# Performance work log

Hardware: AMD Instinct MI355X
Metric: run time of the kernel (lower is better)

The kernel has to match this reference:

```python
import jax, jax.numpy as jnp
import numpy as np


def reference(key, value, time_decay, time_first):
    # key, value: [B, T, H]; time_decay/time_first: [H]
    u = time_first
    w = -jnp.exp(time_decay)
    B, T, H = key.shape

    def step(carry, kv):
        a, b, exponent = carry  # each [B, H]
        kt, vt = kv             # [B, H] each
        # numerically stabilized WKV output at this timestep
        max_e = jnp.maximum(exponent, u + kt)
        wt = jnp.exp(u + kt - max_e)
        scale = jnp.exp(exponent - max_e)
        wkv = (a * scale + wt * vt) / (b * scale + wt)
        # state update with decay w
        max_e2 = jnp.maximum(exponent + w, kt)
        s1 = jnp.exp(exponent + w - max_e2)
        s2 = jnp.exp(kt - max_e2)
        a_new = s1 * a + s2 * vt
        b_new = s1 * b + s2
        return (a_new, b_new, max_e2), wkv

    init = (
        jnp.zeros((B, H), dtype=key.dtype),
        jnp.zeros((B, H), dtype=key.dtype),
        jnp.full((B, H), -jnp.inf, dtype=key.dtype),
    )
    k_t = jnp.transpose(key, (1, 0, 2))    # [T, B, H]
    v_t = jnp.transpose(value, (1, 0, 2))  # [T, B, H]
    _, out = jax.lax.scan(step, init, (k_t, v_t))
    return jnp.transpose(out, (1, 0, 2))   # [B, T, H]


def setup_inputs() -> dict:
    k = jax.random.key(0)
    k1, k2, k3, k4 = jax.random.split(k, 4)
    B, T, H = 8, 2048, 768
    return {
        "key": jax.random.normal(k1, (B, T, H), dtype=jnp.float32),
        "value": jax.random.normal(k2, (B, T, H), dtype=jnp.float32),
        "time_decay": jax.random.normal(k3, (H,), dtype=jnp.float32),
        "time_first": jax.random.normal(k4, (H,), dtype=jnp.float32),
    }
```

## Files before the change

kernel.cpp:

```cpp
#include <hip/hip_runtime.h>
#include <math.h>


#define B_    8
#define T_    2048
#define H_    768
#define H4_   (H_/4)
#define NQ_   8
#define NCB_  32
#define L_    8
#define QLEN_ (NCB_*L_)
#define HS_   (H_/32)
#define HO4_  8
#define NT_   256
#define PAD_  33

#define EXCL_N ((size_t)B_*HS_*NQ_*NCB_*32)
#define TOT_N  ((size_t)B_*HS_*NQ_*32)

__global__ __launch_bounds__(NT_) void wkv_p1(
    const float* __restrict__ key, const float* __restrict__ val,
    const float* __restrict__ time_decay,
    float* __restrict__ ea, float* __restrict__ eb, float* __restrict__ ee,
    float* __restrict__ ta, float* __restrict__ tb, float* __restrict__ te)
{
    __shared__ float sa[NCB_][PAD_];
    __shared__ float sb[NCB_][PAD_];
    __shared__ float se[NCB_][PAD_];

    const int tid = threadIdx.x;
    const int ho4 = tid & (HO4_ - 1);
    const int c   = tid >> 3;
    const int col = ho4 * 4;
    const int hs  = blockIdx.x;
    const int q   = blockIdx.y;
    const int b   = blockIdx.z;
    const int h0  = hs * 32 + col;

    const float4 td4 = *(const float4*)(time_decay + h0);
    float w[4];
    w[0] = -__expf(td4.x); w[1] = -__expf(td4.y);
    w[2] = -__expf(td4.z); w[3] = -__expf(td4.w);

    const int cg = q * NCB_ + c;
    const size_t base = ((size_t)b * T_ + (size_t)cg * L_) * H_ + h0;
    const float4* kp = (const float4*)(key + base);
    const float4* vp = (const float4*)(val + base);

    float4 kr[L_], vr[L_];
#pragma unroll
    for (int t = 0; t < L_; ++t) {
        kr[t] = kp[(size_t)t * H4_];
        vr[t] = vp[(size_t)t * H4_];
    }

    float a[4]  = {0.f, 0.f, 0.f, 0.f};
    float bb[4] = {0.f, 0.f, 0.f, 0.f};
    float e[4]  = {-INFINITY, -INFINITY, -INFINITY, -INFINITY};

#pragma unroll
    for (int t = 0; t < L_; ++t) {
        const float kt[4] = {kr[t].x, kr[t].y, kr[t].z, kr[t].w};
        const float vt[4] = {vr[t].x, vr[t].y, vr[t].z, vr[t].w};
#pragma unroll
        for (int j = 0; j < 4; ++j) {
            const float ew = e[j] + w[j];
            const float m2 = fmaxf(ew, kt[j]);
            const float s1 = __expf(ew - m2);
            const float s2 = __expf(kt[j] - m2);
            a[j]  = fmaf(s1, a[j],  s2 * vt[j]);
            bb[j] = fmaf(s1, bb[j], s2);
            e[j]  = m2;
        }
    }

#pragma unroll
    for (int j = 0; j < 4; ++j) {
        sa[c][col + j] = a[j];
        sb[c][col + j] = bb[j];
        se[c][col + j] = e[j];
    }
    __syncthreads();

#pragma unroll
    for (int s = 0; s < 5; ++s) {
        const int d = 1 << s;
        const bool act = (c >= d);
        float pa[4], pb[4], pe[4];
        if (act) {
#pragma unroll
            for (int j = 0; j < 4; ++j) {
                pa[j] = sa[c - d][col + j];
                pb[j] = sb[c - d][col + j];
                pe[j] = se[c - d][col + j] + w[j] * (float)(L_ * d);
            }
        }
        __syncthreads();
        if (act) {
#pragma unroll
            for (int j = 0; j < 4; ++j) {
                const float m = fmaxf(pe[j], e[j]);
                const float x = __expf(pe[j] - m);
                const float y = __expf(e[j] - m);
                a[j]  = fmaf(pa[j], x, a[j] * y);
                bb[j] = fmaf(pb[j], x, bb[j] * y);
                e[j]  = m;
                sa[c][col + j] = a[j];
                sb[c][col + j] = bb[j];
                se[c][col + j] = e[j];
            }
        }
        __syncthreads();
    }

    float xa[4] = {0.f, 0.f, 0.f, 0.f};
    float xb[4] = {0.f, 0.f, 0.f, 0.f};
    float xe[4] = {-INFINITY, -INFINITY, -INFINITY, -INFINITY};
    if (c > 0) {
#pragma unroll
        for (int j = 0; j < 4; ++j) {
            xa[j] = sa[c - 1][col + j];
            xb[j] = sb[c - 1][col + j];
            xe[j] = se[c - 1][col + j];
        }
    }

    const size_t eoff = ((((size_t)b * HS_ + hs) * NQ_ + q) * NCB_ + c) * 32 + col;
#pragma unroll
    for (int j = 0; j < 4; ++j) {
        ea[eoff + j] = xa[j];
        eb[eoff + j] = xb[j];
        ee[eoff + j] = xe[j];
    }
    if (c == NCB_ - 1) {
        const size_t toff = (((size_t)b * HS_ + hs) * NQ_ + q) * 32 + col;
#pragma unroll
        for (int j = 0; j < 4; ++j) {
            ta[toff + j] = a[j];
            tb[toff + j] = bb[j];
            te[toff + j] = e[j];
        }
    }
}

__global__ __launch_bounds__(NT_) void wkv_p2(
    const float* __restrict__ key, const float* __restrict__ val,
    const float* __restrict__ time_decay, const float* __restrict__ time_first,
    const float* __restrict__ ea, const float* __restrict__ eb,
    const float* __restrict__ ee,
    const float* __restrict__ ta, const float* __restrict__ tb,
    const float* __restrict__ te,
    float* __restrict__ out)
{
    const int tid = threadIdx.x;
    const int ho4 = tid & (HO4_ - 1);
    const int c   = tid >> 3;
    const int col = ho4 * 4;
    const int hs  = blockIdx.x;
    const int q   = blockIdx.y;
    const int b   = blockIdx.z;
    const int h0  = hs * 32 + col;

    const int cg = q * NCB_ + c;
    const size_t base = ((size_t)b * T_ + (size_t)cg * L_) * H_ + h0;
    const float4* kp = (const float4*)(key + base);
    const float4* vp = (const float4*)(val + base);

    float4 kr[L_], vr[L_];
#pragma unroll
    for (int t = 0; t < L_; ++t) {
        kr[t] = kp[(size_t)t * H4_];
        vr[t] = vp[(size_t)t * H4_];
    }

    const float4 td4 = *(const float4*)(time_decay + h0);
    const float4 tf4 = *(const float4*)(time_first + h0);
    float w[4], u[4];
    w[0] = -__expf(td4.x); w[1] = -__expf(td4.y);
    w[2] = -__expf(td4.z); w[3] = -__expf(td4.w);
    u[0] = tf4.x; u[1] = tf4.y; u[2] = tf4.z; u[3] = tf4.w;

    const size_t eoff = ((((size_t)b * HS_ + hs) * NQ_ + q) * NCB_ + c) * 32 + col;
    float ra[4], rb[4], re[4];
#pragma unroll
    for (int j = 0; j < 4; ++j) {
        ra[j] = ea[eoff + j];
        rb[j] = eb[eoff + j];
        re[j] = ee[eoff + j];
    }

    float pa[4] = {0.f, 0.f, 0.f, 0.f};
    float pb[4] = {0.f, 0.f, 0.f, 0.f};
    float pe[4] = {-INFINITY, -INFINITY, -INFINITY, -INFINITY};
    for (int qq = 0; qq < q; ++qq) {
        const size_t toff = (((size_t)b * HS_ + hs) * NQ_ + qq) * 32 + col;
#pragma unroll
        for (int j = 0; j < 4; ++j) {
            const float Ta = ta[toff + j];
            const float Tb = tb[toff + j];
            const float Te = te[toff + j];
            const float sh = pe[j] + w[j] * (float)QLEN_;
            const float m  = fmaxf(sh, Te);
            const float x  = __expf(sh - m);
            const float y  = __expf(Te - m);
            pa[j] = fmaf(pa[j], x, Ta * y);
            pb[j] = fmaf(pb[j], x, Tb * y);
            pe[j] = m;
        }
    }

#pragma unroll
    for (int j = 0; j < 4; ++j) {
        const float sh = pe[j] + w[j] * (float)(c * L_);
        const float m  = fmaxf(sh, re[j]);
        if (m > -INFINITY) {
            const float x = __expf(sh - m);
            const float y = __expf(re[j] - m);
            ra[j] = fmaf(pa[j], x, ra[j] * y);
            rb[j] = fmaf(pb[j], x, rb[j] * y);
            re[j] = m;
        }
    }

    float4* op = (float4*)(out + base);
#pragma unroll
    for (int t = 0; t < L_; ++t) {
        const float kt[4] = {kr[t].x, kr[t].y, kr[t].z, kr[t].w};
        const float vt[4] = {vr[t].x, vr[t].y, vr[t].z, vr[t].w};
        float o[4];
#pragma unroll
        for (int j = 0; j < 4; ++j) {
            const float uk = u[j] + kt[j];
            const float m1 = fmaxf(re[j], uk);
            const float wt = __expf(uk - m1);
            const float sc = __expf(re[j] - m1);
            const float num = fmaf(ra[j], sc, wt * vt[j]);
            const float den = fmaf(rb[j], sc, wt);
            o[j] = __fdividef(num, den);

            const float ew = re[j] + w[j];
            const float m2 = fmaxf(ew, kt[j]);
            const float s1 = __expf(ew - m2);
            const float s2 = __expf(kt[j] - m2);
            ra[j] = fmaf(s1, ra[j], s2 * vt[j]);
            rb[j] = fmaf(s1, rb[j], s2);
            re[j] = m2;
        }
        float4 o4;
        o4.x = o[0]; o4.y = o[1]; o4.z = o[2]; o4.w = o[3];
        op[(size_t)t * H4_] = o4;
    }
}

extern "C" void kernel_launch(void* const* d_in, const int* in_sizes, int n_in,
                              void* d_out, int out_size, void* d_ws, size_t ws_size,
                              hipStream_t stream) {
    const float* key = (const float*)d_in[0];
    const float* val = (const float*)d_in[1];
    const float* td  = (const float*)d_in[2];
    const float* tf  = (const float*)d_in[3];
    float* out = (float*)d_out;

    float* ea = (float*)d_ws;
    float* eb = ea + EXCL_N;
    float* ee = eb + EXCL_N;
    float* ta = ee + EXCL_N;
    float* tb = ta + TOT_N;
    float* te = tb + TOT_N;

    dim3 grid(HS_, NQ_, B_);
    wkv_p1<<<grid, NT_, 0, stream>>>(key, val, td, ea, eb, ee, ta, tb, te);
    wkv_p2<<<grid, NT_, 0, stream>>>(key, val, td, tf, ea, eb, ee, ta, tb, te, out);
}
```

Before: 171.2 us.

## Process two sequence chunks per block and use lgkm-only barriers

Each block now handles two consecutive 256-step chunks instead of one, halving the grid and issuing loads for both chunks up front so the second chunk's global loads overlap the first chunk's compute. __syncthreads is replaced with an inline-asm barrier that waits only on LDS counters, so outstanding global loads need not drain at each scan step. The cost is double the register footprint for the key/value buffers and half as many blocks, which may cut occupancy and parallelism on a 256-CU device.

New measurement: 177.4 us. 1.04x slower.

```diff
diff --git a/kernel.cpp b/kernel.cpp
--- a/kernel.cpp
+++ b/kernel.cpp
@@ -18,42 +18,16 @@
 #define EXCL_N ((size_t)B_*HS_*NQ_*NCB_*32)
 #define TOT_N  ((size_t)B_*HS_*NQ_*32)
 
-__global__ __launch_bounds__(NT_) void wkv_p1(
-    const float* __restrict__ key, const float* __restrict__ val,
-    const float* __restrict__ time_decay,
+#define BAR_LGKM() asm volatile("s_waitcnt lgkmcnt(0)\n\ts_barrier" ::: "memory")
+
+__device__ __forceinline__ void k1_tile(
+    float (*sa)[PAD_], float (*sb)[PAD_], float (*se)[PAD_],
+    const float4* kr, const float4* vr, const float* w,
+    const int c, const int col,
     float* __restrict__ ea, float* __restrict__ eb, float* __restrict__ ee,
-    float* __restrict__ ta, float* __restrict__ tb, float* __restrict__ te)
+    float* __restrict__ ta, float* __restrict__ tb, float* __restrict__ te,
+    const size_t eoff, const size_t toff)
 {
-    __shared__ float sa[NCB_][PAD_];
-    __shared__ float sb[NCB_][PAD_];
-    __shared__ float se[NCB_][PAD_];
-
-    const int tid = threadIdx.x;
-    const int ho4 = tid & (HO4_ - 1);
-    const int c   = tid >> 3;
-    const int col = ho4 * 4;
-    const int hs  = blockIdx.x;
-    const int q   = blockIdx.y;
-    const int b   = blockIdx.z;
-    const int h0  = hs * 32 + col;
-
-    const float4 td4 = *(const float4*)(time_decay + h0);
-    float w[4];
-    w[0] = -__expf(td4.x); w[1] = -__expf(td4.y);
-    w[2] = -__expf(td4.z); w[3] = -__expf(td4.w);
-
-    const int cg = q * NCB_ + c;
-    const size_t base = ((size_t)b * T_ + (size_t)cg * L_) * H_ + h0;
-    const float4* kp = (const float4*)(key + base);
-    const float4* vp = (const float4*)(val + base);
-
-    float4 kr[L_], vr[L_];
-#pragma unroll
-    for (int t = 0; t < L_; ++t) {
-        kr[t] = kp[(size_t)t * H4_];
-        vr[t] = vp[(size_t)t * H4_];
-    }
-
     float a[4]  = {0.f, 0.f, 0.f, 0.f};
     float bb[4] = {0.f, 0.f, 0.f, 0.f};
     float e[4]  = {-INFINITY, -INFINITY, -INFINITY, -INFINITY};
@@ -80,7 +54,7 @@
         sb[c][col + j] = bb[j];
         se[c][col + j] = e[j];
     }
-    __syncthreads();
+    BAR_LGKM();
 
 #pragma unroll
     for (int s = 0; s < 5; ++s) {
@@ -95,7 +69,7 @@
                 pe[j] = se[c - d][col + j] + w[j] * (float)(L_ * d);
             }
         }
-        __syncthreads();
+        BAR_LGKM();
         if (act) {
 #pragma unroll
             for (int j = 0; j < 4; ++j) {
@@ -110,7 +84,7 @@
                 se[c][col + j] = e[j];
             }
         }
-        __syncthreads();
+        BAR_LGKM();
     }
 
     float xa[4] = {0.f, 0.f, 0.f, 0.f};
@@ -124,8 +98,6 @@
             xe[j] = se[c - 1][col + j];
         }
     }
-
-    const size_t eoff = ((((size_t)b * HS_ + hs) * NQ_ + q) * NCB_ + c) * 32 + col;
 #pragma unroll
     for (int j = 0; j < 4; ++j) {
         ea[eoff + j] = xa[j];
@@ -133,13 +105,142 @@
         ee[eoff + j] = xe[j];
     }
     if (c == NCB_ - 1) {
-        const size_t toff = (((size_t)b * HS_ + hs) * NQ_ + q) * 32 + col;
 #pragma unroll
         for (int j = 0; j < 4; ++j) {
             ta[toff + j] = a[j];
             tb[toff + j] = bb[j];
             te[toff + j] = e[j];
         }
+    }
+    BAR_LGKM();
+}
+
+__global__ __launch_bounds__(NT_) void wkv_p1(
+    const float* __restrict__ key, const float* __restrict__ val,
+    const float* __restrict__ time_decay,
+    float* __restrict__ ea, float* __restrict__ eb, float* __restrict__ ee,
+    float* __restrict__ ta, float* __restrict__ tb, float* __restrict__ te)
+{
+    __shared__ float sa[NCB_][PAD_];
+    __shared__ float sb[NCB_][PAD_];
+    __shared__ float se[NCB_][PAD_];
+
+    const int tid = threadIdx.x;
+    const int ho4 = tid & (HO4_ - 1);
+    const int c   = tid >> 3;
+    const int col = ho4 * 4;
+    const int hs  = blockIdx.x;
+    const int q0  = blockIdx.y * 2;
+    const int b   = blockIdx.z;
+    const int h0  = hs * 32 + col;
+
+    const size_t base0 = ((size_t)b * T_ + (size_t)(q0 * NCB_ + c) * L_) * H_ + h0;
+    const size_t base1 = base0 + (size_t)QLEN_ * H_;
+    const float4* kp0 = (const float4*)(key + base0);
+    const float4* vp0 = (const float4*)(val + base0);
+    const float4* kp1 = (const float4*)(key + base1);
+    const float4* vp1 = (const float4*)(val + base1);
+
+    float4 kr0[L_], vr0[L_], kr1[L_], vr1[L_];
+#pragma unroll
+    for (int t = 0; t < L_; ++t) { kr0[t] = kp0[(size_t)t * H4_];
+                                   vr0[t] = vp0[(size_t)t * H4_]; }
+#pragma unroll
+    for (int t = 0; t < L_; ++t) { kr1[t] = kp1[(size_t)t * H4_];
+                                   vr1[t] = vp1[(size_t)t * H4_]; }
+
+    const float4 td4 = *(const float4*)(time_decay + h0);
+    float w[4];
+    w[0] = -__expf(td4.x); w[1] = -__expf(td4.y);
+    w[2] = -__expf(td4.z); w[3] = -__expf(td4.w);
+
+    const size_t eoff0 = ((((size_t)b * HS_ + hs) * NQ_ + q0) * NCB_ + c) * 32 + col;
+    const size_t toff0 = (((size_t)b * HS_ + hs) * NQ_ + q0) * 32 + col;
+
+    k1_tile(sa, sb, se, kr0, vr0, w, c, col, ea, eb, ee, ta, tb, te,
+            eoff0, toff0);
+    k1_tile(sa, sb, se, kr1, vr1, w, c, col, ea, eb, ee, ta, tb, te,
+            eoff0 + (size_t)NCB_ * 32, toff0 + 32);
+}
+
+__device__ __forceinline__ void k2_tile(
+    const float4* kr, const float4* vr,
+    const float* w, const float* u,
+    const int q, const int c, const int col,
+    const float* __restrict__ ea, const float* __restrict__ eb,
+    const float* __restrict__ ee,
+    const float* __restrict__ ta, const float* __restrict__ tb,
+    const float* __restrict__ te,
+    const size_t eoff, const size_t tbase,
+    float4* op)
+{
+    float ra[4], rb[4], re[4];
+#pragma unroll
+    for (int j = 0; j < 4; ++j) {
+        ra[j] = ea[eoff + j];
+        rb[j] = eb[eoff + j];
+        re[j] = ee[eoff + j];
+    }
+
+    float pa[4] = {0.f, 0.f, 0.f, 0.f};
+    float pb[4] = {0.f, 0.f, 0.f, 0.f};
+    float pe[4] = {-INFINITY, -INFINITY, -INFINITY, -INFINITY};
+    for (int qq = 0; qq < q; ++qq) {
+        const size_t toff = tbase + (size_t)qq * 32;
+#pragma unroll
+        for (int j = 0; j < 4; ++j) {
+            const float Ta = ta[toff + j];
+            const float Tb = tb[toff + j];
+            const float Te = te[toff + j];
+            const float sh = pe[j] + w[j] * (float)QLEN_;
+            const float m  = fmaxf(sh, Te);
+            const float x  = __expf(sh - m);
+            const float y  = __expf(Te - m);
+            pa[j] = fmaf(pa[j], x, Ta * y);
+            pb[j] = fmaf(pb[j], x, Tb * y);
+            pe[j] = m;
+        }
+    }
+
+#pragma unroll
+    for (int j = 0; j < 4; ++j) {
+        const float sh = pe[j] + w[j] * (float)(c * L_);
+        const float m  = fmaxf(sh, re[j]);
+        if (m > -INFINITY) {
+            const float x = __expf(sh - m);
+            const float y = __expf(re[j] - m);
+            ra[j] = fmaf(pa[j], x, ra[j] * y);
+            rb[j] = fmaf(pb[j], x, rb[j] * y);
+            re[j] = m;
+        }
+    }
+
+#pragma unroll
+    for (int t = 0; t < L_; ++t) {
+        const float kt[4] = {kr[t].x, kr[t].y, kr[t].z, kr[t].w};
+        const float vt[4] = {vr[t].x, vr[t].y, vr[t].z, vr[t].w};
+        float o[4];
+#pragma unroll
+        for (int j = 0; j < 4; ++j) {
+            const float uk = u[j] + kt[j];
+            const float m1 = fmaxf(re[j], uk);
+            const float wt = __expf(uk - m1);
+            const float sc = __expf(re[j] - m1);
+            const float num = fmaf(ra[j], sc, wt * vt[j]);
+            const float den = fmaf(rb[j], sc, wt);
+            o[j] = __fdividef(num, den);
+
+            const float ew = re[j] + w[j];
+            const float m2 = fmaxf(ew, kt[j]);
+            const float s1 = __expf(ew - m2);
+            const float s2 = __expf(kt[j] - m2);
+            ra[j] = fmaf(s1, ra[j], s2 * vt[j]);
+            rb[j] = fmaf(s1, rb[j], s2);
+            re[j] = m2;
+        }
+        float4 o4;
+        o4.x = o[0]; o4.y = o[1]; o4.z = o[2]; o4.w = o[3];
+        op[(size_t)t * H4_] = o4;
     }
 }
 
@@ -157,21 +258,24 @@
     const int c   = tid >> 3;
     const int col = ho4 * 4;
     const int hs  = blockIdx.x;
-    const int q   = blockIdx.y;
+    const int q0  = blockIdx.y * 2;
     const int b   = blockIdx.z;
     const int h0  = hs * 32 + col;
 
-    const int cg = q * NCB_ + c;
-    const size_t base = ((size_t)b * T_ + (size_t)cg * L_) * H_ + h0;
-    const float4* kp = (const float4*)(key + base);
-    const float4* vp = (const float4*)(val + base);
-
-    float4 kr[L_], vr[L_];
-#pragma unroll
-    for (int t = 0; t < L_; ++t) {
-        kr[t] = kp[(size_t)t * H4_];
-        vr[t] = vp[(size_t)t * H4_];
-    }
+    const size_t base0 = ((size_t)b * T_ + (size_t)(q0 * NCB_ + c) * L_) * H_ + h0;
+    const size_t base1 = base0 + (size_t)QLEN_ * H_;
+    const float4* kp0 = (const float4*)(key + base0);
+    const float4* vp0 = (const float4*)(val + base0);
+    const float4* kp1 = (const float4*)(key + base1);
+    const float4* vp1 = (const float4*)(val + base1);
+
+    float4 kr0[L_], vr0[L_], kr1[L_], vr1[L_];
+#pragma unroll
+    for (int t = 0; t < L_; ++t) { kr0[t] = kp0[(size_t)t * H4_];
+                                   vr0[t] = vp0[(size_t)t * H4_]; }
+#pragma unroll
+    for (int t = 0; t < L_; ++t) { kr1[t] = kp1[(size_t)t * H4_];
+                                   vr1[t] = vp1[(size_t)t * H4_]; }
 
     const float4 td4 = *(const float4*)(time_decay + h0);
     const float4 tf4 = *(const float4*)(time_first + h0);
@@ -180,76 +284,13 @@
     w[2] = -__expf(td4.z); w[3] = -__expf(td4.w);
     u[0] = tf4.x; u[1] = tf4.y; u[2] = tf4.z; u[3] = tf4.w;
 
-    const size_t eoff = ((((size_t)b * HS_ + hs) * NQ_ + q) * NCB_ + c) * 32 + col;
-    float ra[4], rb[4], re[4];
-#pragma unroll
-    for (int j = 0; j < 4; ++j) {
-        ra[j] = ea[eoff + j];
-        rb[j] = eb[eoff + j];
-        re[j] = ee[eoff + j];
-    }
-
-    float pa[4] = {0.f, 0.f, 0.f, 0.f};
-    float pb[4] = {0.f, 0.f, 0.f, 0.f};
-    float pe[4] = {-INFINITY, -INFINITY, -INFINITY, -INFINITY};
-    for (int qq = 0; qq < q; ++qq) {
-        const size_t toff = (((size_t)b * HS_ + hs) * NQ_ + qq) * 32 + col;
-#pragma unroll
-        for (int j = 0; j < 4; ++j) {
-            const float Ta = ta[toff + j];
-            const float Tb = tb[toff + j];
-            const float Te = te[toff + j];
-            const float sh = pe[j] + w[j] * (float)QLEN_;
-            const float m  = fmaxf(sh, Te);
-            const float x  = __expf(sh - m);
-            const float y  = __expf(Te - m);
-            pa[j] = fmaf(pa[j], x, Ta * y);
-            pb[j] = fmaf(pb[j], x, Tb * y);
-            pe[j] = m;
-        }
-    }
-
-#pragma unroll
-    for (int j = 0; j < 4; ++j) {
-        const float sh = pe[j] + w[j] * (float)(c * L_);
-        const float m  = fmaxf(sh, re[j]);
-        if (m > -INFINITY) {
-            const float x = __expf(sh - m);
-            const float y = __expf(re[j] - m);
-            ra[j] = fmaf(pa[j], x, ra[j] * y);
-            rb[j] = fmaf(pb[j], x, rb[j] * y);
-            re[j] = m;
-        }
-    }
-
-    float4* op = (float4*)(out + base);
-#pragma unroll
-    for (int t = 0; t < L_; ++t) {
-        const float kt[4] = {kr[t].x, kr[t].y, kr[t].z, kr[t].w};
-        const float vt[4] = {vr[t].x, vr[t].y, vr[t].z, vr[t].w};
-        float o[4];
-#pragma unroll
-        for (int j = 0; j < 4; ++j) {
-            const float uk = u[j] + kt[j];
-            const float m1 = fmaxf(re[j], uk);
-            const float wt = __expf(uk - m1);
-            const float sc = __expf(re[j] - m1);
-            const float num = fmaf(ra[j], sc, wt * vt[j]);
-            const float den = fmaf(rb[j], sc, wt);
-            o[j] = __fdividef(num, den);
-
-            const float ew = re[j] + w[j];
-            const float m2 = fmaxf(ew, kt[j]);
-            const float s1 = __expf(ew - m2);
-            const float s2 = __expf(kt[j] - m2);
-            ra[j] = fmaf(s1, ra[j], s2 * vt[j]);
-            rb[j] = fmaf(s1, rb[j], s2);
-            re[j] = m2;
-        }
-        float4 o4;
-        o4.x = o[0]; o4.y = o[1]; o4.z = o[2]; o4.w = o[3];
-        op[(size_t)t * H4_] = o4;
-    }
+    const size_t eoff0 = ((((size_t)b * HS_ + hs) * NQ_ + q0) * NCB_ + c) * 32 + col;
+    const size_t tbase = (((size_t)b * HS_ + hs) * NQ_) * 32 + col;
+
+    k2_tile(kr0, vr0, w, u, q0,     c, col, ea, eb, ee, ta, tb, te,
+            eoff0, tbase, (float4*)(out + base0));
+    k2_tile(kr1, vr1, w, u, q0 + 1, c, col, ea, eb, ee, ta, tb, te,
+            eoff0 + (size_t)NCB_ * 32, tbase, (float4*)(out + base1));
 }
 
 extern "C" void kernel_launch(void* const* d_in, const int* in_sizes, int n_in,
@@ -268,7 +309,7 @@
     float* tb = ta + TOT_N;
     float* te = tb + TOT_N;
 
-    dim3 grid(HS_, NQ_, B_);
+    dim3 grid(HS_, NQ_ / 2, B_);
     wkv_p1<<<grid, NT_, 0, stream>>>(key, val, td, ea, eb, ee, ta, tb, te);
     wkv_p2<<<grid, NT_, 0, stream>>>(key, val, td, tf, ea, eb, ee, ta, tb, te, out);
 }
```
